# Kernel optimization log

Measured on AMD Instinct MI355X. Metric: run time of the kernel, lower is better.

## Reference

```python
import jax, jax.numpy as jnp
import numpy as np

R_MAX = 5.0
N_BESSEL = 8
AVG_NEIGH = 32.0
SQRT3 = 3.0 ** 0.5
SQRT2 = 2.0 ** 0.5


def _sph_harm(vec):
    # real spherical harmonics up to l=1, e3nn 'component' normalization:
    # Y0 = 1, Y1 = sqrt(3) * unit_vector
    r = jnp.linalg.norm(vec, axis=-1, keepdims=True)  # [E,1]
    u = vec / (r + 1e-9)
    y0 = jnp.ones_like(r)
    return jnp.concatenate([y0, SQRT3 * u], axis=-1), r[..., 0]  # [E,4],[E]


def _radial(lengths):
    # Bessel radial basis * polynomial cutoff envelope (p=6), as in MACE
    u = lengths / R_MAX
    n = jnp.arange(1, N_BESSEL + 1, dtype=lengths.dtype)
    bess = (2.0 / R_MAX) ** 0.5 * jnp.sin(n * jnp.pi * u[:, None]) / (lengths[:, None] + 1e-9)
    p = 6.0
    env = 1.0 - (p + 1.0) * (p + 2.0) / 2.0 * u ** 6 + p * (p + 2.0) * u ** 7 - p * (p + 1.0) / 2.0 * u ** 8
    env = jnp.where(u < 1.0, env, 0.0)
    return bess * env[:, None]  # [E, N_BESSEL]


def _forward(node_attrs, atom_pos, shifts, W_embed, Wup_s, Wup_v, RW1, RW2, RW3,
             Wout_s, Wout_v, Wsc_s, Wsc_v, P0, P1, Wprod_s, Wprod_v, edge_index):
    N = node_attrs.shape[0]
    sender, receiver = edge_index[0], edge_index[1]
    vec = atom_pos[receiver] - atom_pos[sender] + shifts          # [E,3]
    edge_attrs, lengths = _sph_harm(vec)                          # [E,4],[E]
    edge_feats = _radial(lengths)                                 # [E,8]
    Y0 = edge_attrs[:, 0:1]                                       # [E,1]
    Y1 = edge_attrs[:, 1:4]                                       # [E,3]

    s = node_attrs @ W_embed                                      # node embedding -> [N,C] scalars
    C = s.shape[1]
    v = jnp.zeros((N, C, 3), s.dtype)                             # l=1 features start at zero

    desc = []
    n_layers = Wup_s.shape[0]
    for i in range(n_layers):
        # linear_up: per-l channel mixing
        s_up = s @ Wup_s[i]
        v_up = jnp.einsum('nci,cd->ndi', v, Wup_v[i])
        # radial MLP -> per-edge tensor-product path weights [E,5C]
        h = jax.nn.silu(edge_feats @ RW1[i])
        h = jax.nn.silu(h @ RW2[i])
        w = h @ RW3[i]
        w00, w110, w011, w101, w111 = jnp.split(w, 5, axis=-1)    # each [E,C]
        # gather sender features, CG tensor product with edge SH (paths for lmax=1)
        sj = s_up[sender]                                         # [E,C]
        vj = v_up[sender]                                         # [E,C,3]
        m0 = w00 * sj * Y0 + w110 * jnp.einsum('eci,ei->ec', vj, Y1) / SQRT3
        m1 = (w011[:, :, None] * sj[:, :, None] * Y1[:, None, :]
              + w101[:, :, None] * vj * Y0[:, :, None]
              + w111[:, :, None] * jnp.cross(vj, Y1[:, None, :]) / SQRT2)
        # scatter-reduce messages into receiver nodes
        agg0 = jax.ops.segment_sum(m0, receiver, num_segments=N) / AVG_NEIGH
        agg1 = jax.ops.segment_sum(m1, receiver, num_segments=N) / AVG_NEIGH
        ms = agg0 @ Wout_s[i]
        mv = jnp.einsum('nci,cd->ndi', agg1, Wout_v[i])
        # element-dependent skip connection (node_attrs x node_feats FCTP)
        sc_s = jnp.einsum('nc,nz,zcd->nd', s, node_attrs, Wsc_s[i])
        sc_v = jnp.einsum('nci,nz,zcd->ndi', v, node_attrs, Wsc_v[i])
        # equivariant product basis (symmetric contraction, element-dependent weights)
        p = jnp.einsum('nz,zck->nck', node_attrs, P0[i])          # [N,C,3]
        q = jnp.einsum('nz,zck->nck', node_attrs, P1[i])          # [N,C,2]
        prod_s = p[..., 0] * ms + p[..., 1] * ms * ms + p[..., 2] * jnp.sum(mv * mv, axis=-1)
        prod_v = q[..., 0:1] * mv + q[..., 1:2] * ms[:, :, None] * mv
        s = prod_s @ Wprod_s[i] + sc_s
        v = jnp.einsum('nci,cd->ndi', prod_v, Wprod_v[i]) + sc_v
        # extract_scalar_irreps: first irrep block = l=0 channels
        desc.append(s)
    return jnp.concatenate(desc, axis=-1)                         # [N, n_layers*C]


def setup_inputs() -> dict:
    key = jax.random.key(0)
    ks = jax.random.split(key, 18)
    N, E, C, Z, L, H = 20000, 320000, 64, 10, 2, 64
    species = jax.random.randint(ks[0], (N,), 0, Z)
    node_attrs = jax.nn.one_hot(species, Z, dtype=jnp.float32)
    atom_pos = jax.random.uniform(ks[1], (N, 3), jnp.float32) * 5.0
    edge_index = jax.random.randint(ks[2], (2, E), 0, N)
    shifts = jnp.zeros((E, 3), jnp.float32)

    def w(k, shape, fan_in):
        return jax.random.normal(k, shape, jnp.float32) / np.sqrt(fan_in)

    return {
        'node_attrs': node_attrs,
        'atom_pos': atom_pos,
        'shifts': shifts,
        'W_embed': w(ks[3], (Z, C), Z),
        'Wup_s': w(ks[4], (L, C, C), C),
        'Wup_v': w(ks[5], (L, C, C), C),
        'RW1': w(ks[6], (L, N_BESSEL, H), N_BESSEL),
        'RW2': w(ks[7], (L, H, H), H),
        'RW3': w(ks[8], (L, H, 5 * C), H),
        'Wout_s': w(ks[9], (L, C, C), C),
        'Wout_v': w(ks[10], (L, C, C), C),
        'Wsc_s': w(ks[11], (L, Z, C, C), C),
        'Wsc_v': w(ks[12], (L, Z, C, C), C),
        'P0': w(ks[13], (L, Z, C, 3), 1),
        'P1': w(ks[14], (L, Z, C, 2), 1),
        'Wprod_s': w(ks[15], (L, C, C), C),
        'Wprod_v': w(ks[16], (L, C, C), C),
        'edge_index': edge_index,
    }


def reference(node_attrs, atom_pos, shifts, W_embed, Wup_s, Wup_v, RW1, RW2, RW3,
              Wout_s, Wout_v, Wsc_s, Wsc_v, P0, P1, Wprod_s, Wprod_v, edge_index):
    return _forward(node_attrs, atom_pos, shifts, W_embed, Wup_s, Wup_v, RW1, RW2, RW3,
                    Wout_s, Wout_v, Wsc_s, Wsc_v, P0, P1, Wprod_s, Wprod_v, edge_index)
```

## Files before the change

kernel.cpp:

```cpp
#include <hip/hip_runtime.h>
#include <hip/hip_bf16.h>
#include <hip/hip_fp16.h>

typedef _Float16 half8 __attribute__((ext_vector_type(8)));
typedef float floatx4 __attribute__((ext_vector_type(4)));

union F2H { float f; _Float16 h[2]; };

__device__ __forceinline__ float siluf(float x) {
    return x / (1.0f + __expf(-x));
}

__global__ void k_species(const float* __restrict__ attrs, int* __restrict__ species_o,
                          int* __restrict__ zcount, int N) {
    int n = blockIdx.x * 256 + threadIdx.x;
    if (n >= N) return;
    int z = 0;
    #pragma unroll
    for (int k = 1; k < 10; k++) if (attrs[n * 10 + k] > 0.5f) z = k;
    species_o[n] = z;
    atomicAdd(&zcount[z], 1);
}

__global__ void k_zscan(const int* __restrict__ zcount, int* __restrict__ zcur,
                        int* __restrict__ zstart) {
    if (threadIdx.x == 0) {
        int run = 0;
        for (int z = 0; z < 10; z++) {
            zstart[z] = run;
            zcur[z] = run;
            run += (zcount[z] + 15) & ~15;
        }
        zstart[10] = run;
    }
}

__global__ void k_zperm(const int* __restrict__ species_o, int* __restrict__ zcur,
                        int* __restrict__ perm_n, int* __restrict__ inv_n, int N) {
    int n = blockIdx.x * 256 + threadIdx.x;
    if (n >= N) return;
    int pos = atomicAdd(&zcur[species_o[n]], 1);
    perm_n[pos] = n;
    inv_n[n] = pos;
}

__global__ void k_padmark(const int* __restrict__ zstart, const int* __restrict__ zcur,
                          int* __restrict__ perm_n, int* __restrict__ deg,
                          int* __restrict__ species_s, int Npad) {
    int p = blockIdx.x * 256 + threadIdx.x;
    if (p >= Npad) return;
    deg[p] = 0;
    if (p >= zstart[10]) {
        perm_n[p] = -1;
        species_s[p] = 9;
        return;
    }
    int z = 9;
    #pragma unroll
    for (int q = 0; q < 10; q++) {
        if (p < zstart[q + 1]) { z = q; break; }
    }
    if (p >= zcur[z]) {
        perm_n[p] = -1;
        species_s[p] = z;
    }
}

__global__ void k_init(const int* __restrict__ perm_n, const int* __restrict__ species_o,
                       const float* __restrict__ Wemb, int* __restrict__ species_s,
                       int* __restrict__ origid, float* __restrict__ s,
                       float* __restrict__ v, int Npad) {
    int p = blockIdx.x * 4 + (threadIdx.x >> 6);
    if (p >= Npad) return;
    int lane = threadIdx.x & 63;
    int n = perm_n[p];
    if (n < 0) {
        if (lane == 0) origid[p] = -1;
        s[(size_t)p * 64 + lane] = 0.0f;
        v[(size_t)p * 192 + lane] = 0.0f;
        v[(size_t)p * 192 + 64 + lane] = 0.0f;
        v[(size_t)p * 192 + 128 + lane] = 0.0f;
        return;
    }
    int z = species_o[n];
    if (lane == 0) { species_s[p] = z; origid[p] = n; }
    s[(size_t)p * 64 + lane] = Wemb[z * 64 + lane];
    v[(size_t)p * 192 + lane] = 0.0f;
    v[(size_t)p * 192 + 64 + lane] = 0.0f;
    v[(size_t)p * 192 + 128 + lane] = 0.0f;
}

__global__ void k_hist(const int* __restrict__ ei, const int* __restrict__ inv_n,
                       int* __restrict__ deg, int E) {
    int e = blockIdx.x * 256 + threadIdx.x;
    if (e < E) atomicAdd(&deg[inv_n[ei[E + e]]], 1);
}

__global__ void k_scan(const int* __restrict__ deg, int* __restrict__ rowptr,
                       int* __restrict__ cursor, int N) {
    __shared__ int part[1024];
    int t = threadIdx.x;
    int chunk = (N + 1023) / 1024;
    int lo = t * chunk, hi = min(lo + chunk, N);
    int sum = 0;
    for (int i = lo; i < hi; i++) sum += deg[i];
    part[t] = sum;
    __syncthreads();
    for (int off = 1; off < 1024; off <<= 1) {
        int add = (t >= off) ? part[t - off] : 0;
        __syncthreads();
        part[t] += add;
        __syncthreads();
    }
    int run = (t > 0) ? part[t - 1] : 0;
    for (int i = lo; i < hi; i++) { rowptr[i] = run; cursor[i] = run; run += deg[i]; }
    if (t == 1023) rowptr[N] = part[1023];
}

__global__ void k_eperm(const int* __restrict__ ei, const int* __restrict__ inv_n,
                        int* __restrict__ cursor, int* __restrict__ perm, int E) {
    int e = blockIdx.x * 256 + threadIdx.x;
    if (e < E) {
        int r = inv_n[ei[E + e]];
        int pos = atomicAdd(&cursor[r], 1);
        perm[pos] = e;
    }
}

__global__ void k_geom(const int* __restrict__ ei, const int* __restrict__ perm,
                       const int* __restrict__ inv_n, const float* __restrict__ pos,
                       const float* __restrict__ shifts, float4* __restrict__ geo,
                       _Float16* __restrict__ efh, int* __restrict__ snd_s,
                       int* __restrict__ rcv_s, int E, int Epad, int padnode) {
    int j = blockIdx.x * 256 + threadIdx.x;
    if (j >= Epad) return;
    if (j >= E) {
        geo[j] = make_float4(0.0f, 0.0f, 0.0f, 0.0f);
        snd_s[j] = padnode;
        rcv_s[j] = padnode;
        half8 z8;
        #pragma unroll
        for (int k = 0; k < 8; k++) z8[k] = (_Float16)0.0f;
        *(half8*)(efh + (size_t)j * 8) = z8;
        return;
    }
    int e = perm[j];
    int snd = ei[e], rcv = ei[E + e];
    float dx = pos[rcv * 3 + 0] - pos[snd * 3 + 0] + shifts[e * 3 + 0];
    float dy = pos[rcv * 3 + 1] - pos[snd * 3 + 1] + shifts[e * 3 + 1];
    float dz = pos[rcv * 3 + 2] - pos[snd * 3 + 2] + shifts[e * 3 + 2];
    float r = sqrtf(dx * dx + dy * dy + dz * dz);
    float rin = 1.0f / (r + 1e-9f);
    const float SQ3 = 1.7320508075688772f;
    geo[j] = make_float4(SQ3 * dx * rin, SQ3 * dy * rin, SQ3 * dz * rin, 0.0f);
    snd_s[j] = inv_n[snd];
    rcv_s[j] = inv_n[rcv];
    float u = r * 0.2f;
    float env = 0.0f;
    if (u < 1.0f) {
        float u2 = u * u;
        float u6 = u2 * u2 * u2;
        env = 1.0f - 28.0f * u6 + 48.0f * u6 * u - 21.0f * u6 * u2;
    }
    const float PIF = 3.14159265358979f;
    float x = PIF * u;
    float sp = __sinf(x), cp = __cosf(x);
    float coef = 0.6324555320336759f * rin * env;
    float sm1 = 0.0f, scur = sp, twoc = 2.0f * cp;
    half8 e8;
    #pragma unroll
    for (int k = 0; k < 8; k++) {
        e8[k] = (_Float16)(coef * scur);
        float nxt = twoc * scur - sm1;
        sm1 = scur; scur = nxt;
    }
    *(half8*)(efh + (size_t)j * 8) = e8;
}

__global__ void k_wprep(const float* __restrict__ RW1, const float* __restrict__ RW2,
                        const float* __restrict__ RW3, _Float16* __restrict__ B1f,
                        _Float16* __restrict__ B2f, _Float16* __restrict__ B3f) {
    int lane = threadIdx.x;
    int t = blockIdx.x;
    int layer = t / 52;
    int tt = t % 52;
    int quad = lane >> 4, colx = lane & 15;
    if (tt < 4) {
        int nt = tt;
        const float* W = RW1 + (size_t)layer * 512;
        _Float16* dst = B1f + (size_t)layer * 2048 + ((size_t)nt * 64 + lane) * 8;
        #pragma unroll
        for (int j = 0; j < 8; j++) {
            int k = quad * 8 + j, n = nt * 16 + colx;
            dst[j] = (k < 8) ? (_Float16)W[k * 64 + n] : (_Float16)0.0f;
        }
    } else if (tt < 12) {
        int u = tt - 4;
        int kt = u >> 2, nt = u & 3;
        const float* W = RW2 + (size_t)layer * 4096;
        _Float16* dst = B2f + (size_t)layer * 4096 + (((size_t)kt * 4 + nt) * 64 + lane) * 8;
        #pragma unroll
        for (int j = 0; j < 8; j++) {
            int k = kt * 32 + quad * 8 + j, n = nt * 16 + colx;
            dst[j] = (_Float16)W[k * 64 + n];
        }
    } else {
        int u = tt - 12;
        int kt = u / 20, nt = u % 20;
        const float* W = RW3 + (size_t)layer * 20480;
        _Float16* dst = B3f + (size_t)layer * 20480 + (((size_t)kt * 20 + nt) * 64 + lane) * 8;
        const float inv32 = 1.0f / 32.0f;
        const float is3 = 0.5773502691896258f;
        const float is2 = 0.7071067811865476f;
        #pragma unroll
        for (int j = 0; j < 8; j++) {
            int k = kt * 32 + quad * 8 + j, n = nt * 16 + colx;
            int grp = n >> 6;
            float scale = inv32 * (grp == 1 ? is3 : (grp == 4 ? is2 : 1.0f));
            dst[j] = (_Float16)(W[k * 320 + n] * scale);
        }
    }
}

__global__ void k_wprep_node(const float* __restrict__ Wup_s, const float* __restrict__ Wup_v,
                             const float* __restrict__ Wout_s, const float* __restrict__ Wout_v,
                             const float* __restrict__ Wprod_s, const float* __restrict__ Wprod_v,
                             const float* __restrict__ Wsc_s, const float* __restrict__ Wsc_v,
                             _Float16* __restrict__ Bmats) {
    int mid = blockIdx.x;
    int layer = mid / 26, m = mid % 26;
    const float* src;
    if (m == 0)      src = Wup_s  + (size_t)layer * 4096;
    else if (m == 1) src = Wup_v  + (size_t)layer * 4096;
    else if (m == 2) src = Wout_s + (size_t)layer * 4096;
    else if (m == 3) src = Wout_v + (size_t)layer * 4096;
    else if (m == 4) src = Wprod_s + (size_t)layer * 4096;
    else if (m == 5) src = Wprod_v + (size_t)layer * 4096;
    else if (m < 16) src = Wsc_s + (size_t)layer * 40960 + (size_t)(m - 6) * 4096;
    else             src = Wsc_v + (size_t)layer * 40960 + (size_t)(m - 16) * 4096;
    _Float16* dst = Bmats + (size_t)mid * 4096;
    int lane = threadIdx.x, quad = lane >> 4, colx = lane & 15;
    for (int t = 0; t < 8; t++) {
        int kt = t >> 2, nt = t & 3;
        #pragma unroll
        for (int j = 0; j < 8; j++) {
            int k = kt * 32 + quad * 8 + j, n = nt * 16 + colx;
            dst[(size_t)t * 512 + lane * 8 + j] = (_Float16)src[k * 64 + n];
        }
    }
}

__device__ __forceinline__ half8 loadA(const float* __restrict__ base) {
    half8 a;
    float4 f0 = ((const float4*)base)[0];
    float4 f1 = ((const float4*)base)[1];
    a[0]=(_Float16)f0.x; a[1]=(_Float16)f0.y; a[2]=(_Float16)f0.z; a[3]=(_Float16)f0.w;
    a[4]=(_Float16)f1.x; a[5]=(_Float16)f1.y; a[6]=(_Float16)f1.z; a[7]=(_Float16)f1.w;
    return a;
}

__global__ __launch_bounds__(64, 4)
void k_nodeA(const float* __restrict__ s, const float* __restrict__ v,
             const int* __restrict__ species,
             const _Float16* __restrict__ Bup_s, const _Float16* __restrict__ Bup_v,
             const _Float16* __restrict__ Bsc_s, const _Float16* __restrict__ Bsc_v,
             float2* __restrict__ packh, float2* __restrict__ scph,
             float* __restrict__ agg0, float* __restrict__ agg1, int Npad) {
    const int lane = threadIdx.x & 63;
    const int quad = lane >> 4, col = lane & 15;
    const int n0 = blockIdx.x * 16;
    if (n0 >= Npad) return;

    half8 as[2], av0[2], av1[2], av2[2];
    int node = n0 + col;
    const float* sp = s + (size_t)node * 64;
    const float* vp = v + (size_t)node * 192;
    #pragma unroll
    for (int kt = 0; kt < 2; kt++) {
        int kb = kt * 32 + quad * 8;
        as[kt]  = loadA(sp + kb);
        av0[kt] = loadA(vp + kb);
        av1[kt] = loadA(vp + 64 + kb);
        av2[kt] = loadA(vp + 128 + kb);
    }

    const int z = species[n0];
    const _Float16* Bs = Bsc_s + (size_t)z * 4096;
    const _Float16* Bv = Bsc_v + (size_t)z * 4096;

    #pragma unroll
    for (int nt = 0; nt < 4; nt++) {
        floatx4 cs = {0,0,0,0}, c0 = {0,0,0,0}, c1 = {0,0,0,0}, c2 = {0,0,0,0};
        floatx4 ds = {0,0,0,0}, d0 = {0,0,0,0}, d1 = {0,0,0,0}, d2 = {0,0,0,0};
        #pragma unroll
        for (int kt = 0; kt < 2; kt++) {
            half8 bs = *(const half8*)(Bup_s + (((size_t)kt * 4 + nt) * 64 + lane) * 8);
            half8 bv = *(const half8*)(Bup_v + (((size_t)kt * 4 + nt) * 64 + lane) * 8);
            half8 es = *(const half8*)(Bs + (((size_t)kt * 4 + nt) * 64 + lane) * 8);
            half8 ev = *(const half8*)(Bv + (((size_t)kt * 4 + nt) * 64 + lane) * 8);
            cs = __builtin_amdgcn_mfma_f32_16x16x32_f16(as[kt],  bs, cs, 0, 0, 0);
            c0 = __builtin_amdgcn_mfma_f32_16x16x32_f16(av0[kt], bv, c0, 0, 0, 0);
            c1 = __builtin_amdgcn_mfma_f32_16x16x32_f16(av1[kt], bv, c1, 0, 0, 0);
            c2 = __builtin_amdgcn_mfma_f32_16x16x32_f16(av2[kt], bv, c2, 0, 0, 0);
            ds = __builtin_amdgcn_mfma_f32_16x16x32_f16(as[kt],  es, ds, 0, 0, 0);
            d0 = __builtin_amdgcn_mfma_f32_16x16x32_f16(av0[kt], ev, d0, 0, 0, 0);
            d1 = __builtin_amdgcn_mfma_f32_16x16x32_f16(av1[kt], ev, d1, 0, 0, 0);
            d2 = __builtin_amdgcn_mfma_f32_16x16x32_f16(av2[kt], ev, d2, 0, 0, 0);
        }
        int ch = nt * 16 + col;
        #pragma unroll
        for (int r = 0; r < 4; r++) {
            int n = n0 + quad * 4 + r;
            F2H u1, u2, w1, w2;
            u1.h[0] = (_Float16)cs[r]; u1.h[1] = (_Float16)c0[r];
            u2.h[0] = (_Float16)c1[r]; u2.h[1] = (_Float16)c2[r];
            w1.h[0] = (_Float16)ds[r]; w1.h[1] = (_Float16)d0[r];
            w2.h[0] = (_Float16)d1[r]; w2.h[1] = (_Float16)d2[r];
            packh[(size_t)n * 64 + ch] = make_float2(u1.f, u2.f);
            scph[(size_t)n * 64 + ch]  = make_float2(w1.f, w2.f);
            agg0[(size_t)n * 64 + ch] = 0.0f;
            agg1[(size_t)n * 192 + ch] = 0.0f;
            agg1[(size_t)n * 192 + 64 + ch] = 0.0f;
            agg1[(size_t)n * 192 + 128 + ch] = 0.0f;
        }
    }
}

#define ROWP 72
#define MROW 66

#define MSG_ROW(R, GR, PRV)                                                    \
    {                                                                          \
        F2H u1_, u2_; u1_.f = PRV.x; u2_.f = PRV.y;                            \
        float pvx = (float)u1_.h[0], pvy = (float)u1_.h[1];                    \
        float pvz = (float)u2_.h[0], pvw = (float)u2_.h[1];                    \
        float w00 = acc0[R], w110 = acc1[R], w011 = acc2[R];                   \
        float w101 = acc3[R], w111 = acc4[R];                                  \
        float dvy = pvy * GR.x + pvz * GR.y + pvw * GR.z;                      \
        float m0v = w00 * pvx + w110 * dvy;                                    \
        float cxv = pvz * GR.z - pvw * GR.y;                                   \
        float cyv = pvw * GR.x - pvy * GR.z;                                   \
        float czv = pvy * GR.y - pvz * GR.x;                                   \
        float wps = w011 * pvx;                                                \
        float m1x = wps * GR.x + w101 * pvy + w111 * cxv;                      \
        float m1y = wps * GR.y + w101 * pvz + w111 * cyv;                      \
        float m1z = wps * GR.z + w101 * pvw + w111 * czv;                      \
        F2H o1_, o2_;                                                          \
        o1_.h[0] = (_Float16)m0v; o1_.h[1] = (_Float16)m1x;                    \
        o2_.h[0] = (_Float16)m1y; o2_.h[1] = (_Float16)m1z;                    \
        mt[(wave * 16 + quad * 4 + R) * MROW + CBc] = make_float2(o1_.f, o2_.f); \
    }

#define MSG_ACC(CB, Q, ACC)                                                    \
    {                                                                          \
        half8 b0_ = *(const half8*)(B3f + (((size_t)(0 * 20 + Q * 4 + CB)) * 64 + lane) * 8); \
        half8 b1_ = *(const half8*)(B3f + (((size_t)(1 * 20 + Q * 4 + CB)) * 64 + lane) * 8); \
        ACC = __builtin_amdgcn_mfma_f32_16x16x32_f16(a3f0, b0_, ACC, 0, 0, 0); \
        ACC = __builtin_amdgcn_mfma_f32_16x16x32_f16(a3f1, b1_, ACC, 0, 0, 0); \
    }

#define MSG_CB(CB, P0, P1, P2, P3)                                             \
    {                                                                          \
        floatx4 acc0 = {0,0,0,0}, acc1 = {0,0,0,0}, acc2 = {0,0,0,0};          \
        floatx4 acc3 = {0,0,0,0}, acc4 = {0,0,0,0};                            \
        MSG_ACC(CB, 0, acc0) MSG_ACC(CB, 1, acc1) MSG_ACC(CB, 2, acc2)         \
        MSG_ACC(CB, 3, acc3) MSG_ACC(CB, 4, acc4)                              \
        const int CBc = CB * 16 + col;                                         \
        MSG_ROW(0, gr0, P0) MSG_ROW(1, gr1, P1)                                \
        MSG_ROW(2, gr2, P2) MSG_ROW(3, gr3, P3)                                \
    }

__global__ __launch_bounds__(256, 4)
void k_msg(const _Float16* __restrict__ efh, const float4* __restrict__ geo,
           const int* __restrict__ snd_s, const int* __restrict__ rcv_s,
           const float2* __restrict__ packh,
           const _Float16* __restrict__ B1f, const _Float16* __restrict__ B2f,
           const _Float16* __restrict__ B3f,
           float* __restrict__ agg0, float* __restrict__ agg1) {
    __shared__ float2 mt[64 * MROW];
    _Float16* a2 = (_Float16*)mt;
    _Float16* a3 = (_Float16*)mt + 4608;
    const int tid = threadIdx.x;
    const int lane = tid & 63;
    const int wave = tid >> 6;
    const int quad = lane >> 4;
    const int col = lane & 15;
    const int j0 = blockIdx.x * 64 + wave * 16;

    _Float16* a2w = a2 + wave * 16 * ROWP;
    _Float16* a3w = a3 + wave * 16 * ROWP;

    half8 aef = *(const half8*)(efh + (size_t)(j0 + col) * 8);
    {
        floatx4 c1[4];
        #pragma unroll
        for (int nt = 0; nt < 4; nt++) {
            c1[nt] = (floatx4){0.0f, 0.0f, 0.0f, 0.0f};
            half8 b = *(const half8*)(B1f + ((size_t)nt * 64 + lane) * 8);
            c1[nt] = __builtin_amdgcn_mfma_f32_16x16x32_f16(aef, b, c1[nt], 0, 0, 0);
        }
        #pragma unroll
        for (int nt = 0; nt < 4; nt++)
            #pragma unroll
            for (int r = 0; r < 4; r++)
                a2w[(quad * 4 + r) * ROWP + nt * 16 + col] = (_Float16)siluf(c1[nt][r]);
    }
    __syncthreads();

    {
        half8 af0 = *(const half8*)&a2w[col * ROWP + quad * 8];
        half8 af1 = *(const half8*)&a2w[col * ROWP + 32 + quad * 8];
        floatx4 c2[4];
        #pragma unroll
        for (int nt = 0; nt < 4; nt++) {
            c2[nt] = (floatx4){0.0f, 0.0f, 0.0f, 0.0f};
            half8 b0 = *(const half8*)(B2f + (((size_t)0 * 4 + nt) * 64 + lane) * 8);
            half8 b1 = *(const half8*)(B2f + (((size_t)1 * 4 + nt) * 64 + lane) * 8);
            c2[nt] = __builtin_amdgcn_mfma_f32_16x16x32_f16(af0, b0, c2[nt], 0, 0, 0);
            c2[nt] = __builtin_amdgcn_mfma_f32_16x16x32_f16(af1, b1, c2[nt], 0, 0, 0);
        }
        #pragma unroll
        for (int nt = 0; nt < 4; nt++)
            #pragma unroll
            for (int r = 0; r < 4; r++)
                a3w[(quad * 4 + r) * ROWP + nt * 16 + col] = (_Float16)siluf(c2[nt][r]);
    }
    __syncthreads();

    half8 a3f0 = *(const half8*)&a3w[col * ROWP + quad * 8];
    half8 a3f1 = *(const half8*)&a3w[col * ROWP + 32 + quad * 8];
    __syncthreads();

    const int s0 = snd_s[j0 + quad * 4 + 0];
    const int s1 = snd_s[j0 + quad * 4 + 1];
    const int s2 = snd_s[j0 + quad * 4 + 2];
    const int s3 = snd_s[j0 + quad * 4 + 3];
    const float4 gr0 = geo[j0 + quad * 4 + 0];
    const float4 gr1 = geo[j0 + quad * 4 + 1];
    const float4 gr2 = geo[j0 + quad * 4 + 2];
    const float4 gr3 = geo[j0 + quad * 4 + 3];

    const float2* q0 = packh + (size_t)s0 * 64 + col;
    const float2* q1 = packh + (size_t)s1 * 64 + col;
    const float2* q2 = packh + (size_t)s2 * 64 + col;
    const float2* q3 = packh + (size_t)s3 * 64 + col;
    float2 pp00 = q0[0],  pp01 = q1[0],  pp02 = q2[0],  pp03 = q3[0];
    float2 pp10 = q0[16], pp11 = q1[16], pp12 = q2[16], pp13 = q3[16];
    float2 pp20 = q0[32], pp21 = q1[32], pp22 = q2[32], pp23 = q3[32];
    float2 pp30 = q0[48], pp31 = q1[48], pp32 = q2[48], pp33 = q3[48];

    MSG_CB(0, pp00, pp01, pp02, pp03)
    MSG_CB(1, pp10, pp11, pp12, pp13)
    MSG_CB(2, pp20, pp21, pp22, pp23)
    MSG_CB(3, pp30, pp31, pp32, pp33)

    {
        const int c = lane;
        const int jb = j0;
        float a0 = 0.0f, a1 = 0.0f, a2v = 0.0f, a3v = 0.0f;
        int prev = -1;
        #pragma unroll 4
        for (int i = 0; i < 16; i++) {
            int rr = rcv_s[jb + i];
            float2 mv = mt[(wave * 16 + i) * MROW + c];
            F2H u1, u2; u1.f = mv.x; u2.f = mv.y;
            float m0 = (float)u1.h[0], m1 = (float)u1.h[1];
            float m2 = (float)u2.h[0], m3 = (float)u2.h[1];
            if (rr != prev) {
                if (prev >= 0) {
                    atomicAdd(&agg0[(size_t)prev * 64 + c], a0);
                    atomicAdd(&agg1[(size_t)prev * 192 + c], a1);
                    atomicAdd(&agg1[(size_t)prev * 192 + 64 + c], a2v);
                    atomicAdd(&agg1[(size_t)prev * 192 + 128 + c], a3v);
                }
                a0 = m0; a1 = m1; a2v = m2; a3v = m3;
                prev = rr;
            } else {
                a0 += m0; a1 += m1; a2v += m2; a3v += m3;
            }
        }
        if (prev >= 0) {
            atomicAdd(&agg0[(size_t)prev * 64 + c], a0);
            atomicAdd(&agg1[(size_t)prev * 192 + c], a1);
            atomicAdd(&agg1[(size_t)prev * 192 + 64 + c], a2v);
            atomicAdd(&agg1[(size_t)prev * 192 + 128 + c], a3v);
        }
    }
}

#define ROWPB 72
__global__ __launch_bounds__(64, 4)
void k_nodeB(const float* __restrict__ agg0, const float* __restrict__ agg1,
             const int* __restrict__ species, const int* __restrict__ origid,
             const _Float16* __restrict__ Bout_s, const _Float16* __restrict__ Bout_v,
             const _Float16* __restrict__ Bprod_s, const _Float16* __restrict__ Bprod_v,
             const float* __restrict__ P0l, const float* __restrict__ P1l,
             const float2* __restrict__ scph, float* __restrict__ s,
             float* __restrict__ v, float* __restrict__ out,
             int Npad, int layer, int Ltot) {
    __shared__ _Float16 lds[4 * 16 * ROWPB];
    const int lane = threadIdx.x & 63;
    const int quad = lane >> 4, col = lane & 15;
    const int n0 = blockIdx.x * 16;
    if (n0 >= Npad) return;
    _Float16* lw = lds;

    const int z = species[n0];
    {
        half8 as[2], av0[2], av1[2], av2[2];
        int node = n0 + col;
        const float* ap = agg0 + (size_t)node * 64;
        const float* vp = agg1 + (size_t)node * 192;
        #pragma unroll
        for (int kt = 0; kt < 2; kt++) {
            int kb = kt * 32 + quad * 8;
            as[kt]  = loadA(ap + kb);
            av0[kt] = loadA(vp + kb);
            av1[kt] = loadA(vp + 64 + kb);
            av2[kt] = loadA(vp + 128 + kb);
        }
        #pragma unroll
        for (int nt = 0; nt < 4; nt++) {
            floatx4 cs = {0,0,0,0}, c0 = {0,0,0,0}, c1 = {0,0,0,0}, c2 = {0,0,0,0};
            #pragma unroll
            for (int kt = 0; kt < 2; kt++) {
                half8 bs = *(const half8*)(Bout_s + (((size_t)kt * 4 + nt) * 64 + lane) * 8);
                half8 bv = *(const half8*)(Bout_v + (((size_t)kt * 4 + nt) * 64 + lane) * 8);
                cs = __builtin_amdgcn_mfma_f32_16x16x32_f16(as[kt],  bs, cs, 0, 0, 0);
                c0 = __builtin_amdgcn_mfma_f32_16x16x32_f16(av0[kt], bv, c0, 0, 0, 0);
                c1 = __builtin_amdgcn_mfma_f32_16x16x32_f16(av1[kt], bv, c1, 0, 0, 0);
                c2 = __builtin_amdgcn_mfma_f32_16x16x32_f16(av2[kt], bv, c2, 0, 0, 0);
            }
            int ch = nt * 16 + col;
            const float* p = P0l + ((size_t)z * 64 + ch) * 3;
            const float* q = P1l + ((size_t)z * 64 + ch) * 2;
            float p0 = p[0], p1 = p[1], p2 = p[2];
            float q0 = q[0], q1 = q[1];
            #pragma unroll
            for (int r = 0; r < 4; r++) {
                int nl = quad * 4 + r;
                float msv = cs[r];
                float m0 = c0[r], m1 = c1[r], m2 = c2[r];
                float ps = p0 * msv + p1 * msv * msv + p2 * (m0 * m0 + m1 * m1 + m2 * m2);
                float qq = q0 + q1 * msv;
                lw[0 * 16 * ROWPB + nl * ROWPB + ch] = (_Float16)ps;
                lw[1 * 16 * ROWPB + nl * ROWPB + ch] = (_Float16)(qq * m0);
                lw[2 * 16 * ROWPB + nl * ROWPB + ch] = (_Float16)(qq * m1);
                lw[3 * 16 * ROWPB + nl * ROWPB + ch] = (_Float16)(qq * m2);
            }
        }
    }
    __syncthreads();
    {
        half8 as[2], av0[2], av1[2], av2[2];
        #pragma unroll
        for (int kt = 0; kt < 2; kt++) {
            int kb = kt * 32 + quad * 8;
            as[kt]  = *(const half8*)&lw[0 * 16 * ROWPB + col * ROWPB + kb];
            av0[kt] = *(const half8*)&lw[1 * 16 * ROWPB + col * ROWPB + kb];
            av1[kt] = *(const half8*)&lw[2 * 16 * ROWPB + col * ROWPB + kb];
            av2[kt] = *(const half8*)&lw[3 * 16 * ROWPB + col * ROWPB + kb];
        }
        int og[4];
        #pragma unroll
        for (int r = 0; r < 4; r++) og[r] = origid[n0 + quad * 4 + r];
        #pragma unroll
        for (int nt = 0; nt < 4; nt++) {
            floatx4 cs = {0,0,0,0}, c0 = {0,0,0,0}, c1 = {0,0,0,0}, c2 = {0,0,0,0};
            #pragma unroll
            for (int kt = 0; kt < 2; kt++) {
                half8 bs = *(const half8*)(Bprod_s + (((size_t)kt * 4 + nt) * 64 + lane) * 8);
                half8 bv = *(const half8*)(Bprod_v + (((size_t)kt * 4 + nt) * 64 + lane) * 8);
                cs = __builtin_amdgcn_mfma_f32_16x16x32_f16(as[kt],  bs, cs, 0, 0, 0);
                c0 = __builtin_amdgcn_mfma_f32_16x16x32_f16(av0[kt], bv, c0, 0, 0, 0);
                c1 = __builtin_amdgcn_mfma_f32_16x16x32_f16(av1[kt], bv, c1, 0, 0, 0);
                c2 = __builtin_amdgcn_mfma_f32_16x16x32_f16(av2[kt], bv, c2, 0, 0, 0);
            }
            int ch = nt * 16 + col;
            #pragma unroll
            for (int r = 0; r < 4; r++) {
                int n = n0 + quad * 4 + r;
                float2 scv = scph[(size_t)n * 64 + ch];
                F2H u1, u2; u1.f = scv.x; u2.f = scv.y;
                float sval = cs[r] + (float)u1.h[0];
                s[(size_t)n * 64 + ch] = sval;
                v[(size_t)n * 192 + ch] = c0[r] + (float)u1.h[1];
                v[(size_t)n * 192 + 64 + ch] = c1[r] + (float)u2.h[0];
                v[(size_t)n * 192 + 128 + ch] = c2[r] + (float)u2.h[1];
                if (og[r] >= 0)
                    out[(size_t)og[r] * (Ltot * 64) + layer * 64 + ch] = sval;
            }
        }
    }
}

extern "C" void kernel_launch(void* const* d_in, const int* in_sizes, int n_in,
                              void* d_out, int out_size, void* d_ws, size_t ws_size,
                              hipStream_t stream) {
    const float* node_attrs = (const float*)d_in[0];
    const float* atom_pos   = (const float*)d_in[1];
    const float* shifts     = (const float*)d_in[2];
    const float* W_embed    = (const float*)d_in[3];
    const float* Wup_s      = (const float*)d_in[4];
    const float* Wup_v      = (const float*)d_in[5];
    const float* RW1        = (const float*)d_in[6];
    const float* RW2        = (const float*)d_in[7];
    const float* RW3        = (const float*)d_in[8];
    const float* Wout_s     = (const float*)d_in[9];
    const float* Wout_v     = (const float*)d_in[10];
    const float* Wsc_s      = (const float*)d_in[11];
    const float* Wsc_v      = (const float*)d_in[12];
    const float* P0         = (const float*)d_in[13];
    const float* P1         = (const float*)d_in[14];
    const float* Wprod_s    = (const float*)d_in[15];
    const float* Wprod_v    = (const float*)d_in[16];
    const int*   ei         = (const int*)d_in[17];

    const int N = in_sizes[0] / 10;
    const int E = in_sizes[17] / 2;
    const int L = in_sizes[4] / 4096;
    const int Npad = ((N + 160) + 63) / 64 * 64;
    const int Epad = (E + 63) / 64 * 64;
    float* out = (float*)d_out;

    char* wsb = (char*)d_ws;
    size_t off = 0;
    auto alloci = [&](size_t n) {
        int* p = (int*)(wsb + off);
        off = (off + n * 4 + 255) / 256 * 256;
        return p;
    };
    auto allocf = [&](size_t n) {
        float* p = (float*)(wsb + off);
        off = (off + n * 4 + 255) / 256 * 256;
        return p;
    };
    auto alloch = [&](size_t n) {
        _Float16* p = (_Float16*)(wsb + off);
        off = (off + n * 2 + 255) / 256 * 256;
        return p;
    };
    int* species_o = alloci(N);
    int* species_s = alloci(Npad);
    int* zcount    = alloci(16);
    int* zcur      = alloci(16);
    int* zstart    = alloci(16);
    int* perm_n    = alloci(Npad);
    int* inv_n     = alloci(N);
    int* origid    = alloci(Npad);
    int* deg       = alloci(Npad);
    int* rowptr    = alloci(Npad + 1);
    int* cursor    = alloci(Npad);
    int* perm      = alloci(E);
    int* snd_s     = alloci(Epad);
    int* rcv_s     = alloci(Epad);
    float* s     = allocf((size_t)Npad * 64);
    float* v     = allocf((size_t)Npad * 192);
    float* agg0  = allocf((size_t)Npad * 64);
    float* agg1  = allocf((size_t)Npad * 192);
    float* geo   = allocf((size_t)Epad * 4);
    _Float16* efh = alloch((size_t)Epad * 8);
    float* packh = allocf((size_t)Npad * 128);
    float* scph  = allocf((size_t)Npad * 128);
    _Float16* B1f   = alloch((size_t)L * 2048);
    _Float16* B2f   = alloch((size_t)L * 4096);
    _Float16* B3f   = alloch((size_t)L * 20480);
    _Float16* Bmats = alloch((size_t)L * 26 * 4096);
    (void)n_in; (void)out_size; (void)ws_size;

    const int NT16 = Npad / 16;
    const int NB = (N + 255) / 256;
    const int NPB = (Npad + 255) / 256;
    const int EB = (E + 255) / 256;
    const int EPB = (Epad + 255) / 256;
    const int ET64 = Epad / 64;

    hipMemsetAsync(zcount, 0, 16 * sizeof(int), stream);
    k_species<<<NB, 256, 0, stream>>>(node_attrs, species_o, zcount, N);
    k_zscan<<<1, 64, 0, stream>>>(zcount, zcur, zstart);
    k_zperm<<<NB, 256, 0, stream>>>(species_o, zcur, perm_n, inv_n, N);
    k_padmark<<<NPB, 256, 0, stream>>>(zstart, zcur, perm_n, deg, species_s, Npad);
    k_init<<<(Npad + 3) / 4, 256, 0, stream>>>(perm_n, species_o, W_embed, species_s,
                                               origid, s, v, Npad);
    k_hist<<<EB, 256, 0, stream>>>(ei, inv_n, deg, E);
    k_scan<<<1, 1024, 0, stream>>>(deg, rowptr, cursor, Npad);
    k_eperm<<<EB, 256, 0, stream>>>(ei, inv_n, cursor, perm, E);
    k_geom<<<EPB, 256, 0, stream>>>(ei, perm, inv_n, atom_pos, shifts,
                                    (float4*)geo, efh, snd_s, rcv_s, E, Epad, Npad - 1);
    k_wprep<<<52 * L, 64, 0, stream>>>(RW1, RW2, RW3, B1f, B2f, B3f);
    k_wprep_node<<<26 * L, 64, 0, stream>>>(Wup_s, Wup_v, Wout_s, Wout_v,
                                            Wprod_s, Wprod_v, Wsc_s, Wsc_v, Bmats);

    for (int i = 0; i < L; i++) {
        const _Float16* Bl = Bmats + (size_t)i * 26 * 4096;
        k_nodeA<<<NT16, 64, 0, stream>>>(s, v, species_s,
                                         Bl, Bl + 4096,
                                         Bl + 6 * 4096, Bl + 16 * 4096,
                                         (float2*)packh, (float2*)scph, agg0, agg1, Npad);
        k_msg<<<ET64, 256, 0, stream>>>(efh, (const float4*)geo, snd_s, rcv_s,
                                        (const float2*)packh,
                                        B1f + (size_t)i * 2048, B2f + (size_t)i * 4096,
                                        B3f + (size_t)i * 20480, agg0, agg1);
        k_nodeB<<<NT16, 64, 0, stream>>>(agg0, agg1, species_s, origid,
                                         Bl + 2 * 4096, Bl + 3 * 4096,
                                         Bl + 4 * 4096, Bl + 5 * 4096,
                                         P0 + (size_t)i * 1920, P1 + (size_t)i * 1280,
                                         (const float2*)scph, s, v, out, Npad, i, L);
    }
}
```

Measured before the change: 606.9 us.

## Fuse per-layer node output with next layer's node input and merge setup kernels

Adds k_nodeBA, which takes layer i's product and output result and, in the same block, keeps the updated s and v in shared memory as fp16. It then computes layer i+1's up-projection and self-connection matmuls, and zeroes the aggregation buffers. This removes the global s/v round trip and one launch per layer. The last layer uses a trimmed nodeB that computes only the scalar output. It also merges the species scan and padding-mark kernels into k_zperm and k_painit, merges the two weight-prep kernels into one launch, and adds a sched_barrier in k_msg to pin instruction ordering. The risks are higher register and LDS pressure in the fused kernel, and extra fp16 rounding of s/v before the next layer's matmuls.

```diff
diff --git a/kernel.cpp b/kernel.cpp
--- a/kernel.cpp
+++ b/kernel.cpp
@@ -22,69 +22,53 @@
     atomicAdd(&zcount[z], 1);
 }
 
-__global__ void k_zscan(const int* __restrict__ zcount, int* __restrict__ zcur,
-                        int* __restrict__ zstart) {
-    if (threadIdx.x == 0) {
-        int run = 0;
-        for (int z = 0; z < 10; z++) {
-            zstart[z] = run;
-            zcur[z] = run;
-            run += (zcount[z] + 15) & ~15;
-        }
-        zstart[10] = run;
-    }
-}
-
-__global__ void k_zperm(const int* __restrict__ species_o, int* __restrict__ zcur,
-                        int* __restrict__ perm_n, int* __restrict__ inv_n, int N) {
+__global__ void k_zperm(const int* __restrict__ species_o, const int* __restrict__ zcount,
+                        int* __restrict__ zoff, int* __restrict__ perm_n,
+                        int* __restrict__ inv_n, int N) {
     int n = blockIdx.x * 256 + threadIdx.x;
     if (n >= N) return;
-    int pos = atomicAdd(&zcur[species_o[n]], 1);
+    int z = species_o[n];
+    int start = 0;
+    #pragma unroll
+    for (int q = 0; q < 10; q++) {
+        if (q == z) break;
+        start += (zcount[q] + 15) & ~15;
+    }
+    int pos = start + atomicAdd(&zoff[z], 1);
     perm_n[pos] = n;
     inv_n[n] = pos;
 }
 
-__global__ void k_padmark(const int* __restrict__ zstart, const int* __restrict__ zcur,
-                          int* __restrict__ perm_n, int* __restrict__ deg,
-                          int* __restrict__ species_s, int Npad) {
-    int p = blockIdx.x * 256 + threadIdx.x;
-    if (p >= Npad) return;
-    deg[p] = 0;
-    if (p >= zstart[10]) {
-        perm_n[p] = -1;
-        species_s[p] = 9;
-        return;
-    }
-    int z = 9;
-    #pragma unroll
-    for (int q = 0; q < 10; q++) {
-        if (p < zstart[q + 1]) { z = q; break; }
-    }
-    if (p >= zcur[z]) {
-        perm_n[p] = -1;
-        species_s[p] = z;
-    }
-}
-
-__global__ void k_init(const int* __restrict__ perm_n, const int* __restrict__ species_o,
-                       const float* __restrict__ Wemb, int* __restrict__ species_s,
-                       int* __restrict__ origid, float* __restrict__ s,
-                       float* __restrict__ v, int Npad) {
+__global__ void k_painit(const int* __restrict__ zcount, const int* __restrict__ perm_n,
+                         const int* __restrict__ species_o, const float* __restrict__ Wemb,
+                         int* __restrict__ species_s, int* __restrict__ origid,
+                         int* __restrict__ deg, float* __restrict__ s,
+                         float* __restrict__ v, int Npad) {
     int p = blockIdx.x * 4 + (threadIdx.x >> 6);
     if (p >= Npad) return;
     int lane = threadIdx.x & 63;
-    int n = perm_n[p];
-    if (n < 0) {
-        if (lane == 0) origid[p] = -1;
+    if (lane == 0) deg[p] = 0;
+    int z = -1, run = 0, start = 0, cnt = 0;
+    #pragma unroll
+    for (int q = 0; q < 10; q++) {
+        int c = zcount[q];
+        int sz = (c + 15) & ~15;
+        if (z < 0 && p < run + sz) { z = q; start = run; cnt = c; }
+        run += sz;
+    }
+    bool pad = (z < 0) || (p >= start + cnt);
+    if (pad) {
+        if (lane == 0) { origid[p] = -1; species_s[p] = (z < 0) ? 9 : z; }
         s[(size_t)p * 64 + lane] = 0.0f;
         v[(size_t)p * 192 + lane] = 0.0f;
         v[(size_t)p * 192 + 64 + lane] = 0.0f;
         v[(size_t)p * 192 + 128 + lane] = 0.0f;
         return;
     }
-    int z = species_o[n];
-    if (lane == 0) { species_s[p] = z; origid[p] = n; }
-    s[(size_t)p * 64 + lane] = Wemb[z * 64 + lane];
+    int n = perm_n[p];
+    int zn = species_o[n];
+    if (lane == 0) { species_s[p] = zn; origid[p] = n; }
+    s[(size_t)p * 64 + lane] = Wemb[zn * 64 + lane];
     v[(size_t)p * 192 + lane] = 0.0f;
     v[(size_t)p * 192 + 64 + lane] = 0.0f;
     v[(size_t)p * 192 + 128 + lane] = 0.0f;
@@ -177,75 +161,76 @@
     *(half8*)(efh + (size_t)j * 8) = e8;
 }
 
-__global__ void k_wprep(const float* __restrict__ RW1, const float* __restrict__ RW2,
-                        const float* __restrict__ RW3, _Float16* __restrict__ B1f,
-                        _Float16* __restrict__ B2f, _Float16* __restrict__ B3f) {
+__global__ void k_wprep_all(const float* __restrict__ RW1, const float* __restrict__ RW2,
+                            const float* __restrict__ RW3,
+                            const float* __restrict__ Wup_s, const float* __restrict__ Wup_v,
+                            const float* __restrict__ Wout_s, const float* __restrict__ Wout_v,
+                            const float* __restrict__ Wprod_s, const float* __restrict__ Wprod_v,
+                            const float* __restrict__ Wsc_s, const float* __restrict__ Wsc_v,
+                            _Float16* __restrict__ B1f, _Float16* __restrict__ B2f,
+                            _Float16* __restrict__ B3f, _Float16* __restrict__ Bmats,
+                            int nL52) {
     int lane = threadIdx.x;
-    int t = blockIdx.x;
-    int layer = t / 52;
-    int tt = t % 52;
     int quad = lane >> 4, colx = lane & 15;
-    if (tt < 4) {
-        int nt = tt;
-        const float* W = RW1 + (size_t)layer * 512;
-        _Float16* dst = B1f + (size_t)layer * 2048 + ((size_t)nt * 64 + lane) * 8;
-        #pragma unroll
-        for (int j = 0; j < 8; j++) {
-            int k = quad * 8 + j, n = nt * 16 + colx;
-            dst[j] = (k < 8) ? (_Float16)W[k * 64 + n] : (_Float16)0.0f;
-        }
-    } else if (tt < 12) {
-        int u = tt - 4;
-        int kt = u >> 2, nt = u & 3;
-        const float* W = RW2 + (size_t)layer * 4096;
-        _Float16* dst = B2f + (size_t)layer * 4096 + (((size_t)kt * 4 + nt) * 64 + lane) * 8;
-        #pragma unroll
-        for (int j = 0; j < 8; j++) {
-            int k = kt * 32 + quad * 8 + j, n = nt * 16 + colx;
-            dst[j] = (_Float16)W[k * 64 + n];
+    if (blockIdx.x < nL52) {
+        int t = blockIdx.x;
+        int layer = t / 52;
+        int tt = t % 52;
+        if (tt < 4) {
+            int nt = tt;
+            const float* W = RW1 + (size_t)layer * 512;
+            _Float16* dst = B1f + (size_t)layer * 2048 + ((size_t)nt * 64 + lane) * 8;
+            #pragma unroll
+            for (int j = 0; j < 8; j++) {
+                int k = quad * 8 + j, n = nt * 16 + colx;
+                dst[j] = (k < 8) ? (_Float16)W[k * 64 + n] : (_Float16)0.0f;
+            }
+        } else if (tt < 12) {
+            int u = tt - 4;
+            int kt = u >> 2, nt = u & 3;
+            const float* W = RW2 + (size_t)layer * 4096;
+            _Float16* dst = B2f + (size_t)layer * 4096 + (((size_t)kt * 4 + nt) * 64 + lane) * 8;
+            #pragma unroll
+            for (int j = 0; j < 8; j++) {
+                int k = kt * 32 + quad * 8 + j, n = nt * 16 + colx;
+                dst[j] = (_Float16)W[k * 64 + n];
+            }
+        } else {
+            int u = tt - 12;
+            int kt = u / 20, nt = u % 20;
+            const float* W = RW3 + (size_t)layer * 20480;
+            _Float16* dst = B3f + (size_t)layer * 20480 + (((size_t)kt * 20 + nt) * 64 + lane) * 8;
+            const float inv32 = 1.0f / 32.0f;
+            const float is3 = 0.5773502691896258f;
+            const float is2 = 0.7071067811865476f;
+            #pragma unroll
+            for (int j = 0; j < 8; j++) {
+                int k = kt * 32 + quad * 8 + j, n = nt * 16 + colx;
+                int grp = n >> 6;
+                float scale = inv32 * (grp == 1 ? is3 : (grp == 4 ? is2 : 1.0f));
+                dst[j] = (_Float16)(W[k * 320 + n] * scale);
+            }
         }
     } else {
-        int u = tt - 12;
-        int kt = u / 20, nt = u % 20;
-        const float* W = RW3 + (size_t)layer * 20480;
-        _Float16* dst = B3f + (size_t)layer * 20480 + (((size_t)kt * 20 + nt) * 64 + lane) * 8;
-        const float inv32 = 1.0f / 32.0f;
-        const float is3 = 0.5773502691896258f;
-        const float is2 = 0.7071067811865476f;
-        #pragma unroll
-        for (int j = 0; j < 8; j++) {
-            int k = kt * 32 + quad * 8 + j, n = nt * 16 + colx;
-            int grp = n >> 6;
-            float scale = inv32 * (grp == 1 ? is3 : (grp == 4 ? is2 : 1.0f));
-            dst[j] = (_Float16)(W[k * 320 + n] * scale);
-        }
-    }
-}
-
-__global__ void k_wprep_node(const float* __restrict__ Wup_s, const float* __restrict__ Wup_v,
-                             const float* __restrict__ Wout_s, const float* __restrict__ Wout_v,
-                             const float* __restrict__ Wprod_s, const float* __restrict__ Wprod_v,
-                             const float* __restrict__ Wsc_s, const float* __restrict__ Wsc_v,
-                             _Float16* __restrict__ Bmats) {
-    int mid = blockIdx.x;
-    int layer = mid / 26, m = mid % 26;
-    const float* src;
-    if (m == 0)      src = Wup_s  + (size_t)layer * 4096;
-    else if (m == 1) src = Wup_v  + (size_t)layer * 4096;
-    else if (m == 2) src = Wout_s + (size_t)layer * 4096;
-    else if (m == 3) src = Wout_v + (size_t)layer * 4096;
-    else if (m == 4) src = Wprod_s + (size_t)layer * 4096;
-    else if (m == 5) src = Wprod_v + (size_t)layer * 4096;
-    else if (m < 16) src = Wsc_s + (size_t)layer * 40960 + (size_t)(m - 6) * 4096;
-    else             src = Wsc_v + (size_t)layer * 40960 + (size_t)(m - 16) * 4096;
-    _Float16* dst = Bmats + (size_t)mid * 4096;
-    int lane = threadIdx.x, quad = lane >> 4, colx = lane & 15;
-    for (int t = 0; t < 8; t++) {
-        int kt = t >> 2, nt = t & 3;
-        #pragma unroll
-        for (int j = 0; j < 8; j++) {
-            int k = kt * 32 + quad * 8 + j, n = nt * 16 + colx;
-            dst[(size_t)t * 512 + lane * 8 + j] = (_Float16)src[k * 64 + n];
+        int mid = blockIdx.x - nL52;
+        int layer = mid / 26, m = mid % 26;
+        const float* src;
+        if (m == 0)      src = Wup_s  + (size_t)layer * 4096;
+        else if (m == 1) src = Wup_v  + (size_t)layer * 4096;
+        else if (m == 2) src = Wout_s + (size_t)layer * 4096;
+        else if (m == 3) src = Wout_v + (size_t)layer * 4096;
+        else if (m == 4) src = Wprod_s + (size_t)layer * 4096;
+        else if (m == 5) src = Wprod_v + (size_t)layer * 4096;
+        else if (m < 16) src = Wsc_s + (size_t)layer * 40960 + (size_t)(m - 6) * 4096;
+        else             src = Wsc_v + (size_t)layer * 40960 + (size_t)(m - 16) * 4096;
+        _Float16* dst = Bmats + (size_t)mid * 4096;
+        for (int t = 0; t < 8; t++) {
+            int kt = t >> 2, nt = t & 3;
+            #pragma unroll
+            for (int j = 0; j < 8; j++) {
+                int k = kt * 32 + quad * 8 + j, n = nt * 16 + colx;
+                dst[(size_t)t * 512 + lane * 8 + j] = (_Float16)src[k * 64 + n];
+            }
         }
     }
 }
@@ -448,6 +433,7 @@
     float2 pp10 = q0[16], pp11 = q1[16], pp12 = q2[16], pp13 = q3[16];
     float2 pp20 = q0[32], pp21 = q1[32], pp22 = q2[32], pp23 = q3[32];
     float2 pp30 = q0[48], pp31 = q1[48], pp32 = q2[48], pp33 = q3[48];
+    __builtin_amdgcn_sched_barrier(0);
 
     MSG_CB(0, pp00, pp01, pp02, pp03)
     MSG_CB(1, pp10, pp11, pp12, pp13)
@@ -489,23 +475,25 @@
 }
 
 #define ROWPB 72
+
 __global__ __launch_bounds__(64, 4)
-void k_nodeB(const float* __restrict__ agg0, const float* __restrict__ agg1,
-             const int* __restrict__ species, const int* __restrict__ origid,
-             const _Float16* __restrict__ Bout_s, const _Float16* __restrict__ Bout_v,
-             const _Float16* __restrict__ Bprod_s, const _Float16* __restrict__ Bprod_v,
-             const float* __restrict__ P0l, const float* __restrict__ P1l,
-             const float2* __restrict__ scph, float* __restrict__ s,
-             float* __restrict__ v, float* __restrict__ out,
-             int Npad, int layer, int Ltot) {
+void k_nodeBA(float* __restrict__ agg0, float* __restrict__ agg1,
+              const int* __restrict__ species, const int* __restrict__ origid,
+              const _Float16* __restrict__ Bout_s, const _Float16* __restrict__ Bout_v,
+              const _Float16* __restrict__ Bprod_s, const _Float16* __restrict__ Bprod_v,
+              const float* __restrict__ P0l, const float* __restrict__ P1l,
+              const _Float16* __restrict__ Bup_s, const _Float16* __restrict__ Bup_v,
+              const _Float16* __restrict__ Bsc_s, const _Float16* __restrict__ Bsc_v,
+              float2* __restrict__ scph, float2* __restrict__ packh,
+              float* __restrict__ out, int Npad, int layer, int Ltot) {
     __shared__ _Float16 lds[4 * 16 * ROWPB];
     const int lane = threadIdx.x & 63;
     const int quad = lane >> 4, col = lane & 15;
     const int n0 = blockIdx.x * 16;
     if (n0 >= Npad) return;
     _Float16* lw = lds;
-
     const int z = species[n0];
+
     {
         half8 as[2], av0[2], av1[2], av2[2];
         int node = n0 + col;
@@ -580,13 +568,157 @@
             #pragma unroll
             for (int r = 0; r < 4; r++) {
                 int n = n0 + quad * 4 + r;
+                int nl = quad * 4 + r;
                 float2 scv = scph[(size_t)n * 64 + ch];
                 F2H u1, u2; u1.f = scv.x; u2.f = scv.y;
                 float sval = cs[r] + (float)u1.h[0];
-                s[(size_t)n * 64 + ch] = sval;
-                v[(size_t)n * 192 + ch] = c0[r] + (float)u1.h[1];
-                v[(size_t)n * 192 + 64 + ch] = c1[r] + (float)u2.h[0];
-                v[(size_t)n * 192 + 128 + ch] = c2[r] + (float)u2.h[1];
+                float vx = c0[r] + (float)u1.h[1];
+                float vy = c1[r] + (float)u2.h[0];
+                float vz = c2[r] + (float)u2.h[1];
+                if (og[r] >= 0)
+                    out[(size_t)og[r] * (Ltot * 64) + layer * 64 + ch] = sval;
+                lw[0 * 16 * ROWPB + nl * ROWPB + ch] = (_Float16)sval;
+                lw[1 * 16 * ROWPB + nl * ROWPB + ch] = (_Float16)vx;
+                lw[2 * 16 * ROWPB + nl * ROWPB + ch] = (_Float16)vy;
+                lw[3 * 16 * ROWPB + nl * ROWPB + ch] = (_Float16)vz;
+            }
+        }
+    }
+    __syncthreads();
+    {
+        half8 as[2], av0[2], av1[2], av2[2];
+        #pragma unroll
+        for (int kt = 0; kt < 2; kt++) {
+            int kb = kt * 32 + quad * 8;
+            as[kt]  = *(const half8*)&lw[0 * 16 * ROWPB + col * ROWPB + kb];
+            av0[kt] = *(const half8*)&lw[1 * 16 * ROWPB + col * ROWPB + kb];
+            av1[kt] = *(const half8*)&lw[2 * 16 * ROWPB + col * ROWPB + kb];
+            av2[kt] = *(const half8*)&lw[3 * 16 * ROWPB + col * ROWPB + kb];
+        }
+        const _Float16* Bs = Bsc_s + (size_t)z * 4096;
+        const _Float16* Bv = Bsc_v + (size_t)z * 4096;
+        #pragma unroll
+        for (int nt = 0; nt < 4; nt++) {
+            floatx4 cs = {0,0,0,0}, c0 = {0,0,0,0}, c1 = {0,0,0,0}, c2 = {0,0,0,0};
+            floatx4 ds = {0,0,0,0}, d0 = {0,0,0,0}, d1 = {0,0,0,0}, d2 = {0,0,0,0};
+            #pragma unroll
+            for (int kt = 0; kt < 2; kt++) {
+                half8 bs = *(const half8*)(Bup_s + (((size_t)kt * 4 + nt) * 64 + lane) * 8);
+                half8 bv = *(const half8*)(Bup_v + (((size_t)kt * 4 + nt) * 64 + lane) * 8);
+                half8 es = *(const half8*)(Bs + (((size_t)kt * 4 + nt) * 64 + lane) * 8);
+                half8 ev = *(const half8*)(Bv + (((size_t)kt * 4 + nt) * 64 + lane) * 8);
+                cs = __builtin_amdgcn_mfma_f32_16x16x32_f16(as[kt],  bs, cs, 0, 0, 0);
+                c0 = __builtin_amdgcn_mfma_f32_16x16x32_f16(av0[kt], bv, c0, 0, 0, 0);
+                c1 = __builtin_amdgcn_mfma_f32_16x16x32_f16(av1[kt], bv, c1, 0, 0, 0);
+                c2 = __builtin_amdgcn_mfma_f32_16x16x32_f16(av2[kt], bv, c2, 0, 0, 0);
+                ds = __builtin_amdgcn_mfma_f32_16x16x32_f16(as[kt],  es, ds, 0, 0, 0);
+                d0 = __builtin_amdgcn_mfma_f32_16x16x32_f16(av0[kt], ev, d0, 0, 0, 0);
+                d1 = __builtin_amdgcn_mfma_f32_16x16x32_f16(av1[kt], ev, d1, 0, 0, 0);
+                d2 = __builtin_amdgcn_mfma_f32_16x16x32_f16(av2[kt], ev, d2, 0, 0, 0);
+            }
+            int ch = nt * 16 + col;
+            #pragma unroll
+            for (int r = 0; r < 4; r++) {
+                int n = n0 + quad * 4 + r;
+                F2H u1, u2, w1, w2;
+                u1.h[0] = (_Float16)cs[r]; u1.h[1] = (_Float16)c0[r];
+                u2.h[0] = (_Float16)c1[r]; u2.h[1] = (_Float16)c2[r];
+                w1.h[0] = (_Float16)ds[r]; w1.h[1] = (_Float16)d0[r];
+                w2.h[0] = (_Float16)d1[r]; w2.h[1] = (_Float16)d2[r];
+                packh[(size_t)n * 64 + ch] = make_float2(u1.f, u2.f);
+                scph[(size_t)n * 64 + ch]  = make_float2(w1.f, w2.f);
+                agg0[(size_t)n * 64 + ch] = 0.0f;
+                agg1[(size_t)n * 192 + ch] = 0.0f;
+                agg1[(size_t)n * 192 + 64 + ch] = 0.0f;
+                agg1[(size_t)n * 192 + 128 + ch] = 0.0f;
+            }
+        }
+    }
+}
+
+__global__ __launch_bounds__(64, 4)
+void k_nodeB(const float* __restrict__ agg0, const float* __restrict__ agg1,
+             const int* __restrict__ species, const int* __restrict__ origid,
+             const _Float16* __restrict__ Bout_s, const _Float16* __restrict__ Bout_v,
+             const _Float16* __restrict__ Bprod_s,
+             const float* __restrict__ P0l, const float* __restrict__ P1l,
+             const float2* __restrict__ scph, float* __restrict__ out,
+             int Npad, int layer, int Ltot) {
+    __shared__ _Float16 lds[16 * ROWPB];
+    const int lane = threadIdx.x & 63;
+    const int quad = lane >> 4, col = lane & 15;
+    const int n0 = blockIdx.x * 16;
+    if (n0 >= Npad) return;
+    _Float16* lw = lds;
+
+    const int z = species[n0];
+    {
+        half8 as[2], av0[2], av1[2], av2[2];
+        int node = n0 + col;
+        const float* ap = agg0 + (size_t)node * 64;
+        const float* vp = agg1 + (size_t)node * 192;
+        #pragma unroll
+        for (int kt = 0; kt < 2; kt++) {
+            int kb = kt * 32 + quad * 8;
+            as[kt]  = loadA(ap + kb);
+            av0[kt] = loadA(vp + kb);
+            av1[kt] = loadA(vp + 64 + kb);
+            av2[kt] = loadA(vp + 128 + kb);
+        }
+        #pragma unroll
+        for (int nt = 0; nt < 4; nt++) {
+            floatx4 cs = {0,0,0,0}, c0 = {0,0,0,0}, c1 = {0,0,0,0}, c2 = {0,0,0,0};
+            #pragma unroll
+            for (int kt = 0; kt < 2; kt++) {
+                half8 bs = *(const half8*)(Bout_s + (((size_t)kt * 4 + nt) * 64 + lane) * 8);
+                half8 bv = *(const half8*)(Bout_v + (((size_t)kt * 4 + nt) * 64 + lane) * 8);
+                cs = __builtin_amdgcn_mfma_f32_16x16x32_f16(as[kt],  bs, cs, 0, 0, 0);
+                c0 = __builtin_amdgcn_mfma_f32_16x16x32_f16(av0[kt], bv, c0, 0, 0, 0);
+                c1 = __builtin_amdgcn_mfma_f32_16x16x32_f16(av1[kt], bv, c1, 0, 0, 0);
+                c2 = __builtin_amdgcn_mfma_f32_16x16x32_f16(av2[kt], bv, c2, 0, 0, 0);
+            }
+            int ch = nt * 16 + col;
+            const float* p = P0l + ((size_t)z * 64 + ch) * 3;
+            const float* q = P1l + ((size_t)z * 64 + ch) * 2;
+            float p0 = p[0], p1 = p[1], p2 = p[2];
+            float q0 = q[0], q1 = q[1];
+            (void)q0; (void)q1;
+            #pragma unroll
+            for (int r = 0; r < 4; r++) {
+                int nl = quad * 4 + r;
+                float msv = cs[r];
+                float m0 = c0[r], m1 = c1[r], m2 = c2[r];
+                float ps = p0 * msv + p1 * msv * msv + p2 * (m0 * m0 + m1 * m1 + m2 * m2);
+                lw[nl * ROWPB + ch] = (_Float16)ps;
+            }
+        }
+    }
+    __syncthreads();
+    {
+        half8 as[2];
+        #pragma unroll
+        for (int kt = 0; kt < 2; kt++) {
+            int kb = kt * 32 + quad * 8;
+            as[kt] = *(const half8*)&lw[col * ROWPB + kb];
+        }
+        int og[4];
+        #pragma unroll
+        for (int r = 0; r < 4; r++) og[r] = origid[n0 + quad * 4 + r];
+        #pragma unroll
+        for (int nt = 0; nt < 4; nt++) {
+            floatx4 cs = {0,0,0,0};
+            #pragma unroll
+            for (int kt = 0; kt < 2; kt++) {
+                half8 bs = *(const half8*)(Bprod_s + (((size_t)kt * 4 + nt) * 64 + lane) * 8);
+                cs = __builtin_amdgcn_mfma_f32_16x16x32_f16(as[kt], bs, cs, 0, 0, 0);
+            }
+            int ch = nt * 16 + col;
+            #pragma unroll
+            for (int r = 0; r < 4; r++) {
+                int n = n0 + quad * 4 + r;
+                float2 scv = scph[(size_t)n * 64 + ch];
+                F2H u1; u1.f = scv.x;
+                float sval = cs[r] + (float)u1.h[0];
                 if (og[r] >= 0)
                     out[(size_t)og[r] * (Ltot * 64) + layer * 64 + ch] = sval;
             }
@@ -642,9 +774,8 @@
     };
     int* species_o = alloci(N);
     int* species_s = alloci(Npad);
-    int* zcount    = alloci(16);
-    int* zcur      = alloci(16);
-    int* zstart    = alloci(16);
+    int* zcount    = alloci(32);
+    int* zoff      = zcount + 16;
     int* perm_n    = alloci(Npad);
     int* inv_n     = alloci(N);
     int* origid    = alloci(Npad);
@@ -670,41 +801,52 @@
 
     const int NT16 = Npad / 16;
     const int NB = (N + 255) / 256;
-    const int NPB = (Npad + 255) / 256;
     const int EB = (E + 255) / 256;
     const int EPB = (Epad + 255) / 256;
     const int ET64 = Epad / 64;
 
-    hipMemsetAsync(zcount, 0, 16 * sizeof(int), stream);
+    hipMemsetAsync(zcount, 0, 32 * sizeof(int), stream);
     k_species<<<NB, 256, 0, stream>>>(node_attrs, species_o, zcount, N);
-    k_zscan<<<1, 64, 0, stream>>>(zcount, zcur, zstart);
-    k_zperm<<<NB, 256, 0, stream>>>(species_o, zcur, perm_n, inv_n, N);
-    k_padmark<<<NPB, 256, 0, stream>>>(zstart, zcur, perm_n, deg, species_s, Npad);
-    k_init<<<(Npad + 3) / 4, 256, 0, stream>>>(perm_n, species_o, W_embed, species_s,
-                                               origid, s, v, Npad);
+    k_zperm<<<NB, 256, 0, stream>>>(species_o, zcount, zoff, perm_n, inv_n, N);
+    k_painit<<<(Npad + 3) / 4, 256, 0, stream>>>(zcount, perm_n, species_o, W_embed,
+                                                 species_s, origid, deg, s, v, Npad);
     k_hist<<<EB, 256, 0, stream>>>(ei, inv_n, deg, E);
     k_scan<<<1, 1024, 0, stream>>>(deg, rowptr, cursor, Npad);
     k_eperm<<<EB, 256, 0, stream>>>(ei, inv_n, cursor, perm, E);
     k_geom<<<EPB, 256, 0, stream>>>(ei, perm, inv_n, atom_pos, shifts,
                                     (float4*)geo, efh, snd_s, rcv_s, E, Epad, Npad - 1);
-    k_wprep<<<52 * L, 64, 0, stream>>>(RW1, RW2, RW3, B1f, B2f, B3f);
-    k_wprep_node<<<26 * L, 64, 0, stream>>>(Wup_s, Wup_v, Wout_s, Wout_v,
-                                            Wprod_s, Wprod_v, Wsc_s, Wsc_v, Bmats);
+    k_wprep_all<<<78 * L, 64, 0, stream>>>(RW1, RW2, RW3,
+                                           Wup_s, Wup_v, Wout_s, Wout_v,
+                                           Wprod_s, Wprod_v, Wsc_s, Wsc_v,
+                                           B1f, B2f, B3f, Bmats, 52 * L);
 
     for (int i = 0; i < L; i++) {
         const _Float16* Bl = Bmats + (size_t)i * 26 * 4096;
-        k_nodeA<<<NT16, 64, 0, stream>>>(s, v, species_s,
-                                         Bl, Bl + 4096,
-                                         Bl + 6 * 4096, Bl + 16 * 4096,
-                                         (float2*)packh, (float2*)scph, agg0, agg1, Npad);
+        if (i == 0)
+            k_nodeA<<<NT16, 64, 0, stream>>>(s, v, species_s,
+                                             Bl, Bl + 4096,
+                                             Bl + 6 * 4096, Bl + 16 * 4096,
+                                             (float2*)packh, (float2*)scph, agg0, agg1, Npad);
         k_msg<<<ET64, 256, 0, stream>>>(efh, (const float4*)geo, snd_s, rcv_s,
                                         (const float2*)packh,
                                         B1f + (size_t)i * 2048, B2f + (size_t)i * 4096,
                                         B3f + (size_t)i * 20480, agg0, agg1);
-        k_nodeB<<<NT16, 64, 0, stream>>>(agg0, agg1, species_s, origid,
-                                         Bl + 2 * 4096, Bl + 3 * 4096,
-                                         Bl + 4 * 4096, Bl + 5 * 4096,
-                                         P0 + (size_t)i * 1920, P1 + (size_t)i * 1280,
-                                         (const float2*)scph, s, v, out, Npad, i, L);
-    }
-}
+        if (i + 1 < L) {
+            const _Float16* Bn = Bmats + (size_t)(i + 1) * 26 * 4096;
+            k_nodeBA<<<NT16, 64, 0, stream>>>(agg0, agg1, species_s, origid,
+                                              Bl + 2 * 4096, Bl + 3 * 4096,
+                                              Bl + 4 * 4096, Bl + 5 * 4096,
+                                              P0 + (size_t)i * 1920, P1 + (size_t)i * 1280,
+                                              Bn, Bn + 4096,
+                                              Bn + 6 * 4096, Bn + 16 * 4096,
+                                              (float2*)scph, (float2*)packh,
+                                              out, Npad, i, L);
+        } else {
+            k_nodeB<<<NT16, 64, 0, stream>>>(agg0, agg1, species_s, origid,
+                                             Bl + 2 * 4096, Bl + 3 * 4096,
+                                             Bl + 4 * 4096,
+                                             P0 + (size_t)i * 1920, P1 + (size_t)i * 1280,
+                                             (const float2*)scph, out, Npad, i, L);
+        }
+    }
+}
```

Result: faster. 586.5 us (-3.4%).
